# Performance work log

Measured on AMD Instinct MI355X. Metric: run time of the kernel, lower is better.

The kernel has to match this reference:

```python
import jax, jax.numpy as jnp
import numpy as np

NUM_CLASSES = 2
THRESHOLD = 0.35
NEGPOS_RATIO = 7
VARIANCES = (0.1, 0.2)
B, P, O = 64, 16800, 64  # batch, num_priors, num_objs per image


def point_form(pr):
    # cxcywh -> xyxy
    return jnp.concatenate([pr[:, :2] - pr[:, 2:] / 2, pr[:, :2] + pr[:, 2:] / 2], axis=1)


def jaccard(a, b):
    # a: [A,4] xyxy, b: [Bx,4] xyxy -> IoU [A,Bx]
    lt = jnp.maximum(a[:, None, :2], b[None, :, :2])
    rb = jnp.minimum(a[:, None, 2:], b[None, :, 2:])
    wh = jnp.clip(rb - lt, 0.0)
    inter = wh[..., 0] * wh[..., 1]
    area_a = ((a[:, 2] - a[:, 0]) * (a[:, 3] - a[:, 1]))[:, None]
    area_b = ((b[:, 2] - b[:, 0]) * (b[:, 3] - b[:, 1]))[None, :]
    return inter / (area_a + area_b - inter)


def encode(matched, priors):
    # matched xyxy [P,4], priors cxcywh [P,4]
    g_cxcy = (matched[:, :2] + matched[:, 2:]) / 2 - priors[:, :2]
    g_cxcy = g_cxcy / (VARIANCES[0] * priors[:, 2:])
    g_wh = (matched[:, 2:] - matched[:, :2]) / priors[:, 2:]
    g_wh = jnp.log(g_wh) / VARIANCES[1]
    return jnp.concatenate([g_cxcy, g_wh], axis=1)


def encode_landm(matched, priors):
    # matched [P,10] -> [P,5,2]
    m = matched.reshape(-1, 5, 2)
    g = (m - priors[:, None, :2]) / (VARIANCES[0] * priors[:, None, 2:])
    return g.reshape(-1, 10)


def match_one(truths, labels, landms, priors):
    # truths [O,4], labels [O], landms [O,10]
    overlaps = jaccard(truths, point_form(priors))  # [O,P]
    best_prior_overlap = overlaps.max(axis=1)       # per-gt best IoU
    best_prior_idx = overlaps.argmax(axis=1)
    valid_gt = best_prior_overlap >= 0.2
    best_truth_overlap = overlaps.max(axis=0)       # per-prior best IoU
    best_truth_idx = overlaps.argmax(axis=0)
    # index_fill(2) only for valid gts (best_prior_idx_filter)
    bto = best_truth_overlap.at[best_prior_idx].set(
        jnp.where(valid_gt, 2.0, best_truth_overlap[best_prior_idx]))
    # ensure every gt keeps its best prior
    bti = best_truth_idx.at[best_prior_idx].set(jnp.arange(truths.shape[0]))
    matches = truths[bti]                  # [P,4]
    conf = labels[bti]                     # [P]
    conf = jnp.where(bto < THRESHOLD, 0.0, conf)
    loc = encode(matches, priors)
    landm = encode_landm(landms[bti], priors)
    return loc, conf, landm


def smooth_l1_sum(x, mask):
    ax = jnp.abs(x)
    v = jnp.where(ax < 1.0, 0.5 * ax * ax, ax - 0.5)
    return (v * mask).sum()


def setup_inputs() -> dict:
    key = jax.random.key(0)
    k1, k2, k3, k4, k5, k6, k7, k8 = jax.random.split(key, 8)
    loc_data = jax.random.normal(k1, (B, P, 4), jnp.float32)
    conf_data = jax.random.normal(k2, (B, P, NUM_CLASSES), jnp.float32)
    landm_data = jax.random.normal(k3, (B, P, 10), jnp.float32)
    # priors: cx,cy in (0,1), w,h in (0.02,0.22)
    cxy = jax.random.uniform(k4, (P, 2), jnp.float32)
    wh = jax.random.uniform(k5, (P, 2), jnp.float32) * 0.2 + 0.02
    priors = jnp.concatenate([cxy, wh], axis=1)
    # targets: valid corner boxes + landmarks + label in {1,-1}
    xy1 = jax.random.uniform(k6, (B, O, 2), jnp.float32) * 0.6
    bwh = jax.random.uniform(k7, (B, O, 2), jnp.float32) * 0.3 + 0.05
    boxes = jnp.concatenate([xy1, xy1 + bwh], axis=-1)
    lms = jax.random.uniform(k8, (B, O, 10), jnp.float32)
    lab = jnp.where(jax.random.uniform(jax.random.fold_in(key, 9), (B, O, 1)) < 0.3, -1.0, 1.0)
    targets = jnp.concatenate([boxes, lms, lab], axis=-1)
    return {"loc_data": loc_data, "conf_data": conf_data, "landm_data": landm_data,
            "priors": priors, "targets": targets}


def reference(loc_data, conf_data, landm_data, priors, targets):
    num = loc_data.shape[0]
    num_priors = priors.shape[0]
    truths = targets[:, :, :4]
    landms = targets[:, :, 4:14]
    labels = targets[:, :, -1]
    loc_t, conf_t, landm_t = jax.vmap(match_one, in_axes=(0, 0, 0, None))(
        truths, labels, landms, priors)  # [B,P,4], [B,P], [B,P,10]

    # landmark loss over conf_t > 0
    pos1 = conf_t > 0
    num_pos_landm = pos1.astype(jnp.int32).sum(axis=1, keepdims=True)
    N1 = jnp.maximum(num_pos_landm.sum().astype(jnp.float32), 1.0)
    loss_landm = smooth_l1_sum(landm_data - landm_t, pos1[..., None].astype(landm_data.dtype))

    # localization loss over conf_t != 0 ; conf_t[pos] = 1
    pos = conf_t != 0
    conf_t01 = jnp.where(pos, 1, 0)  # int {0,1}
    loss_l = smooth_l1_sum(loc_data - loc_t, pos[..., None].astype(loc_data.dtype))

    # hard negative mining on per-prior CE loss (global-max log_sum_exp, as in source)
    batch_conf = conf_data.reshape(-1, NUM_CLASSES)
    x_max = batch_conf.max()
    lse = jnp.log(jnp.exp(batch_conf - x_max).sum(axis=1, keepdims=True)) + x_max
    gathered = jnp.take_along_axis(batch_conf, conf_t01.reshape(-1, 1), axis=1)
    loss_c = (lse - gathered).reshape(num, -1)  # [B,P]; positives NOT zeroed (as in source)
    loss_idx = jnp.argsort(-loss_c, axis=1)
    idx_rank = jnp.argsort(loss_idx, axis=1)
    num_pos = pos.astype(jnp.int32).sum(axis=1, keepdims=True)  # [B,1]
    num_neg = jnp.minimum(NEGPOS_RATIO * num_pos, num_priors - 1)
    neg = idx_rank < num_neg  # [B,P]
    neg_pos = pos | neg

    # cross-entropy (sum) over selected pos+neg priors
    logp = jax.nn.log_softmax(conf_data, axis=-1)  # [B,P,C]
    ce = -jnp.take_along_axis(logp, conf_t01[..., None], axis=-1)[..., 0]
    loss_c_final = (ce * neg_pos.astype(ce.dtype)).sum()

    N = jnp.maximum(num_pos.sum().astype(jnp.float32), 1.0)
    return (loss_l / N, loss_c_final / N, loss_landm / N1)
```

## Files before the change

kernel.cpp:

```cpp
#include <hip/hip_runtime.h>
#include <math.h>

#define BN 64
#define PN 16800
#define ON 64
#define THRESH 0.35f
#define NEGPOS 7
#define GX 66
#define NBLK (BN * GX)
#define GXB 17
#define NBT (BN * GXB)
#define PT 4
#define TG 4
#define PSPLIT 2
#define PHALF 8400
#define NBP2 (BN * 16 * PSPLIT)
#define NBINS 4096
#define MAXM 4096
#define TAILT 104

struct GAcc {
  unsigned ticket;
  float sl, slm, sc;
  int np, np1;
  unsigned pad0, pad1;
};

__device__ __forceinline__ unsigned f2key(float f) {
  unsigned u = __float_as_uint(f);
  return (u & 0x80000000u) ? ~u : (u | 0x80000000u);
}
__device__ __forceinline__ float key2f(unsigned k) {
  unsigned u = (k & 0x80000000u) ? (k & 0x7FFFFFFFu) : ~k;
  return __uint_as_float(u);
}
__device__ __forceinline__ float sl1(float d) {
  float a = fabsf(d);
  return (a < 1.f) ? 0.5f * a * a : a - 0.5f;
}

__global__ void k_match2(const float* __restrict__ priors,
                         const float* __restrict__ targets,
                         float* __restrict__ bto, int* __restrict__ bti,
                         unsigned long long* __restrict__ bpp,
                         GAcc* __restrict__ gacc) {
  int bid = blockIdx.x;
  int tid = threadIdx.x;

  if (bid < NBT) {
    int b = bid / GXB;
    int slab = bid - b * GXB;
    int base = slab * 1024 + tid;
    if (bid == 0 && tid < 8) ((unsigned*)gacc)[tid] = 0;

    __shared__ float4 tbox[ON];
    __shared__ float tarea[ON];
    if (tid < ON) {
      const float* tg = &targets[((long)b * ON + tid) * 15];
      float4 bx = make_float4(tg[0], tg[1], tg[2], tg[3]);
      tbox[tid] = bx;
      tarea[tid] = (bx.z - bx.x) * (bx.w - bx.y);
    }
    __syncthreads();

    float px1[PT], py1[PT], px2[PT], py2[PT], ab[PT];
    bool val[PT];
#pragma unroll
    for (int i = 0; i < PT; i++) {
      int p = base + 256 * i;
      val[i] = p < PN;
      float4 pr = reinterpret_cast<const float4*>(priors)[val[i] ? p : base];
      px1[i] = pr.x - pr.z * 0.5f; py1[i] = pr.y - pr.w * 0.5f;
      px2[i] = pr.x + pr.z * 0.5f; py2[i] = pr.y + pr.w * 0.5f;
      ab[i] = (px2[i] - px1[i]) * (py2[i] - py1[i]);
    }
    float bi[PT], bu[PT]; int id[PT];
#pragma unroll
    for (int i = 0; i < PT; i++) { bi[i] = -1.f; bu[i] = 1.f; id[i] = 0; }

#pragma unroll 4
    for (int t = 0; t < ON; t++) {
      float4 a = tbox[t];
      float aa = tarea[t];
#pragma unroll
      for (int i = 0; i < PT; i++) {
        float lx = fmaxf(a.x, px1[i]), ly = fmaxf(a.y, py1[i]);
        float rx = fminf(a.z, px2[i]), ry = fminf(a.w, py2[i]);
        float w = fmaxf(rx - lx, 0.f), h = fmaxf(ry - ly, 0.f);
        float inter = w * h;
        float uni = aa + ab[i] - inter;
        if (inter * bu[i] > bi[i] * uni) { bi[i] = inter; bu[i] = uni; id[i] = t; }
      }
    }
#pragma unroll
    for (int i = 0; i < PT; i++) {
      if (val[i]) {
        int p = base + 256 * i;
        bto[(long)b * PN + p] = bi[i] / bu[i];
        bti[(long)b * PN + p] = id[i];
      }
    }
  } else {
    int id2 = bid - NBT;
    int b = id2 >> 5;
    int rest = id2 & 31;
    int g = rest >> 1;
    int h = rest & 1;
    int t0 = g * TG;
    float ax1[TG], ay1[TG], ax2[TG], ay2[TG], area_a[TG];
#pragma unroll
    for (int i = 0; i < TG; i++) {
      const float* tg = &targets[((long)b * ON + t0 + i) * 15];
      ax1[i] = tg[0]; ay1[i] = tg[1]; ax2[i] = tg[2]; ay2[i] = tg[3];
      area_a[i] = (ax2[i] - ax1[i]) * (ay2[i] - ay1[i]);
    }
    float bi[TG], bu[TG]; int bp[TG];
#pragma unroll
    for (int i = 0; i < TG; i++) { bi[i] = -1.f; bu[i] = 1.f; bp[i] = 0x7FFFFFFF; }
    int pend = (h + 1) * PHALF;
    for (int p = h * PHALF + tid; p < pend; p += 256) {
      float4 pr = reinterpret_cast<const float4*>(priors)[p];
      float px1 = pr.x - pr.z * 0.5f, py1 = pr.y - pr.w * 0.5f;
      float px2 = pr.x + pr.z * 0.5f, py2 = pr.y + pr.w * 0.5f;
      float area_b = (px2 - px1) * (py2 - py1);
#pragma unroll
      for (int i = 0; i < TG; i++) {
        float lx = fmaxf(ax1[i], px1), ly = fmaxf(ay1[i], py1);
        float rx = fminf(ax2[i], px2), ry = fminf(ay2[i], py2);
        float w = fmaxf(rx - lx, 0.f), h2 = fmaxf(ry - ly, 0.f);
        float inter = w * h2;
        float uni = area_a[i] + area_b - inter;
        if (inter * bu[i] > bi[i] * uni) { bi[i] = inter; bu[i] = uni; bp[i] = p; }
      }
    }
#pragma unroll
    for (int off = 1; off < 64; off <<= 1) {
#pragma unroll
      for (int i = 0; i < TG; i++) {
        float oi = __shfl_xor(bi[i], off), ou = __shfl_xor(bu[i], off);
        int op = __shfl_xor(bp[i], off);
        float a = oi * bu[i], c = bi[i] * ou;
        if (a > c || (a == c && op < bp[i])) { bi[i] = oi; bu[i] = ou; bp[i] = op; }
      }
    }
    __shared__ float si[TG][4], su[TG][4];
    __shared__ int spx[TG][4];
    int w = tid >> 6;
    if ((tid & 63) == 0) {
#pragma unroll
      for (int i = 0; i < TG; i++) { si[i][w] = bi[i]; su[i][w] = bu[i]; spx[i][w] = bp[i]; }
    }
    __syncthreads();
    if (tid < TG) {
      float fi = si[tid][0], fu = su[tid][0]; int fp = spx[tid][0];
      for (int ww = 1; ww < 4; ww++) {
        float a = si[tid][ww] * fu, c = fi * su[tid][ww];
        if (a > c || (a == c && spx[tid][ww] < fp)) { fi = si[tid][ww]; fu = su[tid][ww]; fp = spx[tid][ww]; }
      }
      float q = fi / fu;
      unsigned long long key = ((unsigned long long)f2key(q) << 32) | (unsigned)(~fp);
      bpp[((long)b * ON + t0 + tid) * PSPLIT + h] = key;
    }
  }
}

__global__ void k_encode(const float* __restrict__ loc_data,
                         const float* __restrict__ conf_data,
                         const float* __restrict__ landm_data,
                         const float* __restrict__ priors,
                         const float* __restrict__ targets,
                         const float* __restrict__ bto, const int* __restrict__ bti,
                         const unsigned long long* __restrict__ bpp,
                         float* __restrict__ lossc, unsigned char* __restrict__ posf,
                         float* __restrict__ part_l, float* __restrict__ part_lm,
                         int* __restrict__ np_part, int* __restrict__ np1_part) {
  int b = blockIdx.y;
  int p = blockIdx.x * 256 + threadIdx.x;
  int bid = b * GX + blockIdx.x;
  __shared__ float4 tgs4[ON * 15 / 4];
  __shared__ int ovr[256];
  float* tgs = (float*)tgs4;
  if (threadIdx.x < ON * 15 / 4)
    tgs4[threadIdx.x] = reinterpret_cast<const float4*>(targets + (long)b * ON * 15)[threadIdx.x];
  ovr[threadIdx.x] = -1;
  __syncthreads();
  if (threadIdx.x < ON) {
    int t = threadIdx.x;
    unsigned long long v0 = bpp[((long)b * ON + t) * PSPLIT];
    unsigned long long v1 = bpp[((long)b * ON + t) * PSPLIT + 1];
    unsigned long long best = v0 > v1 ? v0 : v1;
    float q = key2f((unsigned)(best >> 32));
    int qp = (int)(~(unsigned)best);
    int s0 = blockIdx.x * 256;
    if (qp >= s0 && qp < s0 + 256) {
      int valid = (q >= 0.2f) ? 1 : 0;
      atomicMax(&ovr[qp - s0], (t << 1) | valid);
    }
  }
  __syncthreads();

  float sum_l = 0.f, sum_lm = 0.f;
  int cp = 0, cp1 = 0;
  if (p < PN) {
    int t = bti[b * PN + p];
    float ov = bto[b * PN + p];
    int o = ovr[threadIdx.x];
    if (o >= 0) { t = o >> 1; if (o & 1) ov = 2.0f; }
    const float* tg = &tgs[t * 15];
    float label = tg[14];
    bool pos = ov >= THRESH;
    bool pos1 = pos && (label > 0.f);
    float4 pr = reinterpret_cast<const float4*>(priors)[p];
    if (pos) {
      float rz = 1.0f / pr.z, rw = 1.0f / pr.w;
      float m0 = tg[0], m1 = tg[1], m2 = tg[2], m3 = tg[3];
      float g0 = ((m0 + m2) * 0.5f - pr.x) * rz * 10.f;
      float g1 = ((m1 + m3) * 0.5f - pr.y) * rw * 10.f;
      float g2 = __logf((m2 - m0) * rz) * 5.f;
      float g3 = __logf((m3 - m1) * rw) * 5.f;
      const float* ld = &loc_data[((long)b * PN + p) * 4];
      sum_l = sl1(ld[0] - g0) + sl1(ld[1] - g1) + sl1(ld[2] - g2) + sl1(ld[3] - g3);
      cp = 1;
      if (pos1) {
        const float* lm = &landm_data[((long)b * PN + p) * 10];
#pragma unroll
        for (int i = 0; i < 5; i++) {
          float gx = (tg[4 + 2 * i] - pr.x) * rz * 10.f;
          float gy = (tg[5 + 2 * i] - pr.y) * rw * 10.f;
          sum_lm += sl1(lm[2 * i] - gx) + sl1(lm[2 * i + 1] - gy);
        }
        cp1 = 1;
      }
    }
    float2 c2 = reinterpret_cast<const float2*>(conf_data)[(long)b * PN + p];
    float m = fmaxf(c2.x, c2.y);
    float lse = m + __logf(__expf(c2.x - m) + __expf(c2.y - m));
    lossc[b * PN + p] = lse - (pos ? c2.y : c2.x);
    posf[b * PN + p] = pos ? 1 : 0;
  }
  for (int off = 32; off; off >>= 1) {
    sum_l += __shfl_down(sum_l, off);
    sum_lm += __shfl_down(sum_lm, off);
    cp += __shfl_down(cp, off);
    cp1 += __shfl_down(cp1, off);
  }
  __shared__ float sl4[4], slm4[4];
  __shared__ int sp4[4], sp14[4];
  int w = threadIdx.x >> 6;
  if ((threadIdx.x & 63) == 0) { sl4[w] = sum_l; slm4[w] = sum_lm; sp4[w] = cp; sp14[w] = cp1; }
  __syncthreads();
  if (threadIdx.x == 0) {
    part_l[bid] = sl4[0] + sl4[1] + sl4[2] + sl4[3];
    part_lm[bid] = slm4[0] + slm4[1] + slm4[2] + slm4[3];
    np_part[bid] = sp4[0] + sp4[1] + sp4[2] + sp4[3];
    np1_part[bid] = sp14[0] + sp14[1] + sp14[2] + sp14[3];
  }
}

__global__ void __launch_bounds__(1024) k_select(const float* __restrict__ lossc,
                                                 const unsigned char* __restrict__ posf,
                                                 const int* __restrict__ np_part,
                                                 const int* __restrict__ np1_part,
                                                 const float* __restrict__ part_l,
                                                 const float* __restrict__ part_lm,
                                                 GAcc* __restrict__ gacc,
                                                 float* __restrict__ out) {
  int b = blockIdx.x;
  int tid = threadIdx.x;
  int lane = tid & 63;
  int wv = tid >> 6;
  __shared__ unsigned hist[NBINS];
  __shared__ unsigned wtot[16];
  __shared__ float resv[MAXM];
  __shared__ int residx[MAXM];
  __shared__ int s_np, s_B, s_kp;
  __shared__ unsigned s_mc;
  const float* row = &lossc[(long)b * PN];
  const unsigned char* prow = &posf[(long)b * PN];

  if (tid == 0) s_np = 0;
  for (int i = tid; i < NBINS; i += 1024) hist[i] = 0;
  __syncthreads();
  if (tid < GX) atomicAdd(&s_np, np_part[b * GX + tid]);

  const float4* rf4 = reinterpret_cast<const float4*>(row);
  const uint4* pw4 = reinterpret_cast<const uint4*>(prow);
  bool hasTail = tid < TAILT;
  float vm[16];
  float vt[4];
  {
    float4 L0 = rf4[tid * 4], L1 = rf4[tid * 4 + 1], L2 = rf4[tid * 4 + 2], L3 = rf4[tid * 4 + 3];
    vm[0] = L0.x; vm[1] = L0.y; vm[2] = L0.z; vm[3] = L0.w;
    vm[4] = L1.x; vm[5] = L1.y; vm[6] = L1.z; vm[7] = L1.w;
    vm[8] = L2.x; vm[9] = L2.y; vm[10] = L2.z; vm[11] = L2.w;
    vm[12] = L3.x; vm[13] = L3.y; vm[14] = L3.z; vm[15] = L3.w;
  }
  unsigned pmask = 0;
  {
    uint4 W = pw4[tid];
    unsigned w0 = W.x, w1 = W.y, w2 = W.z, w3 = W.w;
#pragma unroll
    for (int j = 0; j < 4; j++) {
      pmask |= ((w0 >> (8 * j)) & 1u) << j;
      pmask |= ((w1 >> (8 * j)) & 1u) << (4 + j);
      pmask |= ((w2 >> (8 * j)) & 1u) << (8 + j);
      pmask |= ((w3 >> (8 * j)) & 1u) << (12 + j);
    }
  }
  unsigned tmask = 0;
  if (hasTail) {
    float4 Lt = rf4[4096 + tid];
    vt[0] = Lt.x; vt[1] = Lt.y; vt[2] = Lt.z; vt[3] = Lt.w;
    unsigned Wt = reinterpret_cast<const unsigned*>(prow)[4096 + tid];
#pragma unroll
    for (int j = 0; j < 4; j++) tmask |= ((Wt >> (8 * j)) & 1u) << j;
  } else {
    vt[0] = vt[1] = vt[2] = vt[3] = -1.f;
  }
  int bm[16], bt4[4];
#pragma unroll
  for (int j = 0; j < 16; j++) {
    int q = (int)(vm[j] * 256.0f);
    bm[j] = q < 0 ? 0 : (q > NBINS - 1 ? NBINS - 1 : q);
  }
#pragma unroll
  for (int j = 0; j < 4; j++) {
    int q = (int)(vt[j] * 256.0f);
    bt4[j] = q < 0 ? 0 : (q > NBINS - 1 ? NBINS - 1 : q);
  }
  __syncthreads();
  int np = s_np;
  int k = NEGPOS * np;
  if (k > PN - 1) k = PN - 1;
  bool haveNeg = (k > 0);

  int B = NBINS, kp = 0, m = 0;
  bool allB = false, fallback = false;
  if (haveNeg) {
#pragma unroll
    for (int j = 0; j < 16; j++) atomicAdd(&hist[bm[j]], 1u);
    if (hasTail) {
#pragma unroll
      for (int j = 0; j < 4; j++) atomicAdd(&hist[bt4[j]], 1u);
    }
    __syncthreads();
    int t4 = tid * 4;
    unsigned h0 = hist[t4], h1 = hist[t4 + 1], h2 = hist[t4 + 2], h3 = hist[t4 + 3];
    unsigned th = h0 + h1 + h2 + h3;
    unsigned v = th;
#pragma unroll
    for (int off = 1; off < 64; off <<= 1) {
      unsigned tv = (unsigned)__shfl_down((int)v, off);
      if (lane + off < 64) v += tv;
    }
    if (lane == 0) wtot[wv] = v;
    __syncthreads();
    unsigned add = 0;
    for (int w2 = wv + 1; w2 < 16; w2++) add += wtot[w2];
    unsigned S_t = v + add;
    unsigned S_next = S_t - th;
    if (S_t >= (unsigned)k && S_next < (unsigned)k) {
      unsigned run = S_next; int Bl; unsigned kpl;
      if (run + h3 >= (unsigned)k) { Bl = t4 + 3; kpl = k - run; }
      else { run += h3;
        if (run + h2 >= (unsigned)k) { Bl = t4 + 2; kpl = k - run; }
        else { run += h2;
          if (run + h1 >= (unsigned)k) { Bl = t4 + 1; kpl = k - run; }
          else { run += h1; Bl = t4; kpl = k - run; } } }
      s_B = Bl; s_kp = (int)kpl;
    }
    __syncthreads();
    B = s_B; kp = s_kp; m = (int)hist[B];
    allB = (kp == m);
    fallback = (!allB && m > MAXM);
  }

  float acc = 0.f;
  if (haveNeg && !allB && !fallback) {
    if (tid == 0) s_mc = 0;
    __syncthreads();
#pragma unroll
    for (int j = 0; j < 16; j++) {
      if (bm[j] == B) {
        unsigned slot = atomicAdd(&s_mc, 1u);
        resv[slot] = vm[j];
        residx[slot] = (tid * 16 + j) | (((pmask >> j) & 1u) ? 0x40000000 : 0);
      }
    }
    if (hasTail) {
#pragma unroll
      for (int j = 0; j < 4; j++) {
        if (bt4[j] == B) {
          unsigned slot = atomicAdd(&s_mc, 1u);
          resv[slot] = vt[j];
          residx[slot] = (16384 + tid * 4 + j) | (((tmask >> j) & 1u) ? 0x40000000 : 0);
        }
      }
    }
    __syncthreads();
    for (int i = tid; i < m; i += 1024) {
      float vi = resv[i];
      int pk = residx[i];
      int ii = pk & 0x3FFFFFFF;
      bool posi = (pk & 0x40000000) != 0;
      int rank = 0;
      for (int j = 0; j < m; j++) {
        float vj = resv[j];
        int ij = residx[j] & 0x3FFFFFFF;
        rank += (vj > vi || (vj == vi && ij < ii)) ? 1 : 0;
      }
      if (rank < kp && !posi) acc += vi;
    }
  }

  unsigned T = 0, R = 0, C = 0;
  if (fallback) {
    __shared__ unsigned s_lo, s_hi, fcnt[16];
    if (tid == 0) { s_lo = 0u; s_hi = 0xFFFFFFFFu; }
    __syncthreads();
    for (int it = 0; it < 32; it++) {
      unsigned lo = s_lo, hi = s_hi;
      unsigned mid = lo + ((hi - lo) >> 1) + ((hi - lo) & 1u);
      unsigned c = 0;
#pragma unroll
      for (int j = 0; j < 16; j++) c += (f2key(vm[j]) >= mid) ? 1u : 0u;
      if (hasTail) {
#pragma unroll
        for (int j = 0; j < 4; j++) c += (f2key(vt[j]) >= mid) ? 1u : 0u;
      }
#pragma unroll
      for (int o = 32; o; o >>= 1) c += (unsigned)__shfl_down((int)c, o);
      if (lane == 0) fcnt[wv] = c;
      __syncthreads();
      if (tid == 0) {
        unsigned tot = 0;
        for (int i = 0; i < 16; i++) tot += fcnt[i];
        if (tot >= (unsigned)k) s_lo = mid; else s_hi = mid - 1;
      }
      __syncthreads();
      if (s_lo >= s_hi) break;
    }
    T = s_lo;
    unsigned cg = 0, ce = 0;
#pragma unroll
    for (int j = 0; j < 16; j++) {
      unsigned key = f2key(vm[j]);
      cg += (key > T) ? 1u : 0u;
      ce += (key == T) ? 1u : 0u;
    }
    if (hasTail) {
#pragma unroll
      for (int j = 0; j < 4; j++) {
        unsigned key = f2key(vt[j]);
        cg += (key > T) ? 1u : 0u;
        ce += (key == T) ? 1u : 0u;
      }
    }
#pragma unroll
    for (int o = 32; o; o >>= 1) {
      cg += (unsigned)__shfl_down((int)cg, o);
      ce += (unsigned)__shfl_down((int)ce, o);
    }
    if (lane == 0) { fcnt[wv] = cg; wtot[wv] = ce; }
    __syncthreads();
    if (tid == 0) {
      unsigned tg2 = 0, te = 0;
      for (int i = 0; i < 16; i++) { tg2 += fcnt[i]; te += wtot[i]; }
      fcnt[0] = tg2; wtot[0] = te;
    }
    __syncthreads();
    C = wtot[0];
    R = (unsigned)k - fcnt[0];
    if (C != R && tid < 64) {
      unsigned running = 0;
      for (int base2 = 0; base2 < PN; base2 += 64) {
        int p = base2 + tid;
        bool tie = false, pos = false;
        float v2 = 0.f;
        if (p < PN) { v2 = row[p]; tie = (f2key(v2) == T); pos = prow[p] != 0; }
        unsigned long long mm = __ballot(tie);
        if (tie) {
          unsigned rank = running + (unsigned)__popcll(mm & ((1ull << tid) - 1));
          if (rank < R && !pos) acc += v2;
        }
        running += (unsigned)__popcll(mm);
      }
    }
  }

  unsigned ptc = 0;
#pragma unroll
  for (int j = 0; j < 16; j++) {
    float v2 = vm[j];
    bool pos = (pmask >> j) & 1u;
    if (pos) acc += v2;
    else if (haveNeg) {
      if (!fallback) {
        if (bm[j] > B || (bm[j] == B && allB)) acc += v2;
      } else {
        if (f2key(v2) > T) acc += v2;
      }
    }
    if (fallback && pos && f2key(v2) == T) ptc++;
  }
  if (hasTail) {
#pragma unroll
    for (int j = 0; j < 4; j++) {
      float v2 = vt[j];
      bool pos = (tmask >> j) & 1u;
      if (pos) acc += v2;
      else if (haveNeg) {
        if (!fallback) {
          if (bt4[j] > B || (bt4[j] == B && allB)) acc += v2;
        } else {
          if (f2key(v2) > T) acc += v2;
        }
      }
      if (fallback && pos && f2key(v2) == T) ptc++;
    }
  }
  for (int o = 32; o; o >>= 1) {
    acc += __shfl_down(acc, o);
    ptc += __shfl_down(ptc, o);
  }
  __shared__ float wsum[16];
  __shared__ unsigned wpt[16];
  if (lane == 0) { wsum[wv] = acc; wpt[wv] = ptc; }
  __syncthreads();

  __shared__ float s_rsl, s_rslm;
  __shared__ int s_rnp1;
  if (tid == 0) { s_rsl = 0.f; s_rslm = 0.f; s_rnp1 = 0; }
  __syncthreads();
  if (tid < GX) {
    atomicAdd(&s_rsl, part_l[b * GX + tid]);
    atomicAdd(&s_rslm, part_lm[b * GX + tid]);
    atomicAdd(&s_rnp1, np1_part[b * GX + tid]);
  }
  __syncthreads();

  if (tid == 0) {
    float tot = 0.f; unsigned pt = 0;
    for (int i = 0; i < 16; i++) { tot += wsum[i]; pt += wpt[i]; }
    if (fallback && C == R) tot += (float)(C - pt) * key2f(T);
    atomicAdd(&gacc->sc, tot);
    atomicAdd(&gacc->sl, s_rsl);
    atomicAdd(&gacc->slm, s_rslm);
    atomicAdd(&gacc->np, np);
    atomicAdd(&gacc->np1, s_rnp1);
  }
  __threadfence();
  __shared__ int lastF;
  if (tid == 0) lastF = (atomicAdd(&gacc->ticket, 1u) == (unsigned)(BN - 1)) ? 1 : 0;
  __syncthreads();
  if (lastF && tid == 0) {
    __threadfence();
    float sl = atomicAdd(&gacc->sl, 0.f);
    float slm = atomicAdd(&gacc->slm, 0.f);
    float sc = atomicAdd(&gacc->sc, 0.f);
    int tnp = atomicAdd(&gacc->np, 0);
    int tnp1 = atomicAdd(&gacc->np1, 0);
    float N = fmaxf((float)tnp, 1.f);
    float N1 = fmaxf((float)tnp1, 1.f);
    out[0] = sl / N;
    out[1] = sc / N;
    out[2] = slm / N1;
  }
}

extern "C" void kernel_launch(void* const* d_in, const int* in_sizes, int n_in,
                              void* d_out, int out_size, void* d_ws, size_t ws_size,
                              hipStream_t stream) {
  const float* loc_data = (const float*)d_in[0];
  const float* conf_data = (const float*)d_in[1];
  const float* landm_data = (const float*)d_in[2];
  const float* priors = (const float*)d_in[3];
  const float* targets = (const float*)d_in[4];
  float* out = (float*)d_out;

  char* ws = (char*)d_ws;
  const size_t SZ = (size_t)BN * PN * 4;
  size_t off = 0;
  float* lossc = (float*)(ws + off); off += SZ;
  float* bto = (float*)(ws + off); off += SZ;
  int* bti = (int*)(ws + off); off += SZ;
  unsigned char* posf = (unsigned char*)(ws + off); off += (size_t)BN * PN;
  off = (off + 15) & ~(size_t)15;
  unsigned long long* bpp = (unsigned long long*)(ws + off);
  off += (size_t)BN * ON * PSPLIT * 8;
  float* part_l = (float*)(ws + off); off += NBLK * 4;
  float* part_lm = (float*)(ws + off); off += NBLK * 4;
  int* np_part = (int*)(ws + off); off += NBLK * 4;
  int* np1_part = (int*)(ws + off); off += NBLK * 4;
  GAcc* gacc = (GAcc*)(ws + off); off += sizeof(GAcc);

  dim3 gbp(GX, BN);

  k_match2<<<NBT + NBP2, 256, 0, stream>>>(priors, targets, bto, bti, bpp, gacc);
  k_encode<<<gbp, 256, 0, stream>>>(loc_data, conf_data, landm_data, priors, targets,
                                    bto, bti, bpp, lossc, posf,
                                    part_l, part_lm, np_part, np1_part);
  k_select<<<BN, 1024, 0, stream>>>(lossc, posf, np_part, np1_part, part_l, part_lm,
                                    gacc, out);
}
```

Baseline: 208.8 us.

## Bin priors into a spatial grid to prune IoU matching candidates

Adds a single-block prior sort into a 16x16 grid by center, per-image cell-to-target overlap masks, and a matching kernel that only evaluates IoU for gt/prior pairs in nearby cells. The per-prior best-truth result is packed into one byte (target id plus positive flag) instead of separate float and int arrays, which cuts global traffic. This removes most of the dense O×P IoU work but adds two extra serial launches, one of them a single-block kernel. It also relies on grid bounds from the maximum prior half-size and uses wave-wide mask unions, so some wavefronts may still scan many targets.

```diff
diff --git a/kernel.cpp b/kernel.cpp
--- a/kernel.cpp
+++ b/kernel.cpp
@@ -8,13 +8,9 @@
 #define NEGPOS 7
 #define GX 66
 #define NBLK (BN * GX)
-#define GXB 17
-#define NBT (BN * GXB)
-#define PT 4
-#define TG 4
-#define PSPLIT 2
-#define PHALF 8400
-#define NBP2 (BN * 16 * PSPLIT)
+#define NBP 1024
+#define NBTT (BN * GX)
+#define NCELL 256
 #define NBINS 4096
 #define MAXM 4096
 #define TAILT 104
@@ -39,127 +35,187 @@
   return (a < 1.f) ? 0.5f * a * a : a - 0.5f;
 }
 
-__global__ void k_match2(const float* __restrict__ priors,
-                         const float* __restrict__ targets,
-                         float* __restrict__ bto, int* __restrict__ bti,
-                         unsigned long long* __restrict__ bpp,
-                         GAcc* __restrict__ gacc) {
+__global__ void __launch_bounds__(1024) k_sort(const float* __restrict__ priors,
+                                               float4* __restrict__ sbox,
+                                               int* __restrict__ sorig,
+                                               int* __restrict__ scell,
+                                               int* __restrict__ inv,
+                                               int* __restrict__ cellOff,
+                                               unsigned* __restrict__ gmax,
+                                               GAcc* __restrict__ gacc) {
+  __shared__ unsigned cnt[NCELL];
+  __shared__ unsigned cur[NCELL];
+  __shared__ unsigned tmp[NCELL];
+  int tid = threadIdx.x;
+  if (tid < NCELL) cnt[tid] = 0;
+  if (tid == 0) { gmax[0] = 0u; gmax[1] = 0u; }
+  if (tid < 8) ((unsigned*)gacc)[tid] = 0;
+  __syncthreads();
+  float mw = 0.f, mh = 0.f;
+  for (int p = tid; p < PN; p += 1024) {
+    float4 pr = reinterpret_cast<const float4*>(priors)[p];
+    int cx = (int)(pr.x * 16.f); cx = cx < 0 ? 0 : (cx > 15 ? 15 : cx);
+    int cy = (int)(pr.y * 16.f); cy = cy < 0 ? 0 : (cy > 15 ? 15 : cy);
+    atomicAdd(&cnt[cy * 16 + cx], 1u);
+    mw = fmaxf(mw, pr.z * 0.5f);
+    mh = fmaxf(mh, pr.w * 0.5f);
+  }
+#pragma unroll
+  for (int off = 32; off; off >>= 1) {
+    mw = fmaxf(mw, __shfl_xor(mw, off));
+    mh = fmaxf(mh, __shfl_xor(mh, off));
+  }
+  if ((tid & 63) == 0) {
+    atomicMax(&gmax[0], __float_as_uint(mw));
+    atomicMax(&gmax[1], __float_as_uint(mh));
+  }
+  __syncthreads();
+  if (tid < NCELL) tmp[tid] = cnt[tid];
+  __syncthreads();
+  for (int off = 1; off < NCELL; off <<= 1) {
+    unsigned v = 0;
+    if (tid < NCELL && tid >= off) v = tmp[tid - off];
+    __syncthreads();
+    if (tid < NCELL) tmp[tid] += v;
+    __syncthreads();
+  }
+  if (tid < NCELL) {
+    unsigned excl = tmp[tid] - cnt[tid];
+    cur[tid] = excl;
+    cellOff[tid] = (int)excl;
+    if (tid == NCELL - 1) cellOff[NCELL] = (int)tmp[tid];
+  }
+  __syncthreads();
+  for (int p = tid; p < PN; p += 1024) {
+    float4 pr = reinterpret_cast<const float4*>(priors)[p];
+    int cx = (int)(pr.x * 16.f); cx = cx < 0 ? 0 : (cx > 15 ? 15 : cx);
+    int cy = (int)(pr.y * 16.f); cy = cy < 0 ? 0 : (cy > 15 ? 15 : cy);
+    int cell = cy * 16 + cx;
+    int s = (int)atomicAdd(&cur[cell], 1u);
+    float px1 = pr.x - pr.z * 0.5f, py1 = pr.y - pr.w * 0.5f;
+    float px2 = pr.x + pr.z * 0.5f, py2 = pr.y + pr.w * 0.5f;
+    sbox[s] = make_float4(px1, py1, px2, py2);
+    sorig[s] = p;
+    scell[s] = cell;
+    inv[p] = s;
+  }
+}
+
+__global__ void k_masks(const float* __restrict__ targets,
+                        const unsigned* __restrict__ gmax,
+                        unsigned long long* __restrict__ tmask) {
+  int b = blockIdx.x;
+  int tid = threadIdx.x;
+  __shared__ float4 tb[ON];
+  if (tid < ON) {
+    const float* tg = &targets[((long)b * ON + tid) * 15];
+    tb[tid] = make_float4(tg[0], tg[1], tg[2], tg[3]);
+  }
+  __syncthreads();
+  float MW = __uint_as_float(gmax[0]), MH = __uint_as_float(gmax[1]);
+  int cx = tid & 15, cy = tid >> 4;
+  float x0 = (float)(cx - 1) * 0.0625f - MW, x1 = (float)(cx + 2) * 0.0625f + MW;
+  float y0 = (float)(cy - 1) * 0.0625f - MH, y1 = (float)(cy + 2) * 0.0625f + MH;
+  unsigned long long m = 0ull;
+  for (int t = 0; t < ON; t++) {
+    float4 a = tb[t];
+    if (x0 < a.z && x1 > a.x && y0 < a.w && y1 > a.y) m |= (1ull << t);
+  }
+  tmask[b * NCELL + tid] = m;
+}
+
+__global__ void k_pair(const float* __restrict__ targets,
+                       const float4* __restrict__ sbox,
+                       const int* __restrict__ sorig,
+                       const int* __restrict__ scell,
+                       const int* __restrict__ cellOff,
+                       const unsigned* __restrict__ gmax,
+                       const unsigned long long* __restrict__ tmask,
+                       unsigned char* __restrict__ btpack,
+                       unsigned long long* __restrict__ bpp) {
   int bid = blockIdx.x;
   int tid = threadIdx.x;
 
-  if (bid < NBT) {
-    int b = bid / GXB;
-    int slab = bid - b * GXB;
-    int base = slab * 1024 + tid;
-    if (bid == 0 && tid < 8) ((unsigned*)gacc)[tid] = 0;
-
-    __shared__ float4 tbox[ON];
-    __shared__ float tarea[ON];
+  if (bid < NBP) {
+    int lane = tid & 63, wv = tid >> 6;
+    int b = bid >> 4;
+    int t = ((bid & 15) << 2) + wv;
+    const float* tg = &targets[((long)b * ON + t) * 15];
+    float ax1 = tg[0], ay1 = tg[1], ax2 = tg[2], ay2 = tg[3];
+    float aa = (ax2 - ax1) * (ay2 - ay1);
+    float MW = __uint_as_float(gmax[0]), MH = __uint_as_float(gmax[1]);
+    int xlo = (int)floorf((ax1 - MW) * 16.f) - 1; xlo = xlo < 0 ? 0 : (xlo > 15 ? 15 : xlo);
+    int xhi = (int)floorf((ax2 + MW) * 16.f) + 1; xhi = xhi < 0 ? 0 : (xhi > 15 ? 15 : xhi);
+    int ylo = (int)floorf((ay1 - MH) * 16.f) - 1; ylo = ylo < 0 ? 0 : (ylo > 15 ? 15 : ylo);
+    int yhi = (int)floorf((ay2 + MH) * 16.f) + 1; yhi = yhi < 0 ? 0 : (yhi > 15 ? 15 : yhi);
+    float bi = 0.f, bu = 1.f; int bp = 0;
+    for (int cy = ylo; cy <= yhi; cy++) {
+      int s0 = cellOff[cy * 16 + xlo];
+      int s1 = cellOff[cy * 16 + xhi + 1];
+      for (int s = s0 + lane; s < s1; s += 64) {
+        float4 pr = sbox[s];
+        int op = sorig[s];
+        float ab2 = (pr.z - pr.x) * (pr.w - pr.y);
+        float lx = fmaxf(ax1, pr.x), ly = fmaxf(ay1, pr.y);
+        float rx = fminf(ax2, pr.z), ry = fminf(ay2, pr.w);
+        float w = fmaxf(rx - lx, 0.f), h = fmaxf(ry - ly, 0.f);
+        float inter = w * h;
+        float uni = aa + ab2 - inter;
+        float A = inter * bu, C = bi * uni;
+        if (A > C || (A == C && op < bp)) { bi = inter; bu = uni; bp = op; }
+      }
+    }
+#pragma unroll
+    for (int off = 1; off < 64; off <<= 1) {
+      float oi = __shfl_xor(bi, off), ou = __shfl_xor(bu, off);
+      int op = __shfl_xor(bp, off);
+      float A = oi * bu, C = bi * ou;
+      if (A > C || (A == C && op < bp)) { bi = oi; bu = ou; bp = op; }
+    }
+    if (lane == 0) {
+      float q = bi / bu;
+      bpp[(long)b * ON + t] = ((unsigned long long)f2key(q) << 32) | (unsigned)(~bp);
+    }
+  } else {
+    int id2 = bid - NBP;
+    int b = id2 / GX;
+    int slab = id2 - b * GX;
+    int s = slab * 256 + tid;
+    bool valid = s < PN;
+    int sc = valid ? s : PN - 1;
+    __shared__ float4 tb[ON];
+    __shared__ float ta[ON];
     if (tid < ON) {
       const float* tg = &targets[((long)b * ON + tid) * 15];
       float4 bx = make_float4(tg[0], tg[1], tg[2], tg[3]);
-      tbox[tid] = bx;
-      tarea[tid] = (bx.z - bx.x) * (bx.w - bx.y);
-    }
-    __syncthreads();
-
-    float px1[PT], py1[PT], px2[PT], py2[PT], ab[PT];
-    bool val[PT];
-#pragma unroll
-    for (int i = 0; i < PT; i++) {
-      int p = base + 256 * i;
-      val[i] = p < PN;
-      float4 pr = reinterpret_cast<const float4*>(priors)[val[i] ? p : base];
-      px1[i] = pr.x - pr.z * 0.5f; py1[i] = pr.y - pr.w * 0.5f;
-      px2[i] = pr.x + pr.z * 0.5f; py2[i] = pr.y + pr.w * 0.5f;
-      ab[i] = (px2[i] - px1[i]) * (py2[i] - py1[i]);
-    }
-    float bi[PT], bu[PT]; int id[PT];
-#pragma unroll
-    for (int i = 0; i < PT; i++) { bi[i] = -1.f; bu[i] = 1.f; id[i] = 0; }
-
-#pragma unroll 4
-    for (int t = 0; t < ON; t++) {
-      float4 a = tbox[t];
-      float aa = tarea[t];
-#pragma unroll
-      for (int i = 0; i < PT; i++) {
-        float lx = fmaxf(a.x, px1[i]), ly = fmaxf(a.y, py1[i]);
-        float rx = fminf(a.z, px2[i]), ry = fminf(a.w, py2[i]);
-        float w = fmaxf(rx - lx, 0.f), h = fmaxf(ry - ly, 0.f);
-        float inter = w * h;
-        float uni = aa + ab[i] - inter;
-        if (inter * bu[i] > bi[i] * uni) { bi[i] = inter; bu[i] = uni; id[i] = t; }
-      }
-    }
-#pragma unroll
-    for (int i = 0; i < PT; i++) {
-      if (val[i]) {
-        int p = base + 256 * i;
-        bto[(long)b * PN + p] = bi[i] / bu[i];
-        bti[(long)b * PN + p] = id[i];
-      }
-    }
-  } else {
-    int id2 = bid - NBT;
-    int b = id2 >> 5;
-    int rest = id2 & 31;
-    int g = rest >> 1;
-    int h = rest & 1;
-    int t0 = g * TG;
-    float ax1[TG], ay1[TG], ax2[TG], ay2[TG], area_a[TG];
-#pragma unroll
-    for (int i = 0; i < TG; i++) {
-      const float* tg = &targets[((long)b * ON + t0 + i) * 15];
-      ax1[i] = tg[0]; ay1[i] = tg[1]; ax2[i] = tg[2]; ay2[i] = tg[3];
-      area_a[i] = (ax2[i] - ax1[i]) * (ay2[i] - ay1[i]);
-    }
-    float bi[TG], bu[TG]; int bp[TG];
-#pragma unroll
-    for (int i = 0; i < TG; i++) { bi[i] = -1.f; bu[i] = 1.f; bp[i] = 0x7FFFFFFF; }
-    int pend = (h + 1) * PHALF;
-    for (int p = h * PHALF + tid; p < pend; p += 256) {
-      float4 pr = reinterpret_cast<const float4*>(priors)[p];
-      float px1 = pr.x - pr.z * 0.5f, py1 = pr.y - pr.w * 0.5f;
-      float px2 = pr.x + pr.z * 0.5f, py2 = pr.y + pr.w * 0.5f;
-      float area_b = (px2 - px1) * (py2 - py1);
-#pragma unroll
-      for (int i = 0; i < TG; i++) {
-        float lx = fmaxf(ax1[i], px1), ly = fmaxf(ay1[i], py1);
-        float rx = fminf(ax2[i], px2), ry = fminf(ay2[i], py2);
-        float w = fmaxf(rx - lx, 0.f), h2 = fmaxf(ry - ly, 0.f);
-        float inter = w * h2;
-        float uni = area_a[i] + area_b - inter;
-        if (inter * bu[i] > bi[i] * uni) { bi[i] = inter; bu[i] = uni; bp[i] = p; }
-      }
-    }
-#pragma unroll
-    for (int off = 1; off < 64; off <<= 1) {
-#pragma unroll
-      for (int i = 0; i < TG; i++) {
-        float oi = __shfl_xor(bi[i], off), ou = __shfl_xor(bu[i], off);
-        int op = __shfl_xor(bp[i], off);
-        float a = oi * bu[i], c = bi[i] * ou;
-        if (a > c || (a == c && op < bp[i])) { bi[i] = oi; bu[i] = ou; bp[i] = op; }
-      }
-    }
-    __shared__ float si[TG][4], su[TG][4];
-    __shared__ int spx[TG][4];
-    int w = tid >> 6;
-    if ((tid & 63) == 0) {
-#pragma unroll
-      for (int i = 0; i < TG; i++) { si[i][w] = bi[i]; su[i][w] = bu[i]; spx[i][w] = bp[i]; }
-    }
-    __syncthreads();
-    if (tid < TG) {
-      float fi = si[tid][0], fu = su[tid][0]; int fp = spx[tid][0];
-      for (int ww = 1; ww < 4; ww++) {
-        float a = si[tid][ww] * fu, c = fi * su[tid][ww];
-        if (a > c || (a == c && spx[tid][ww] < fp)) { fi = si[tid][ww]; fu = su[tid][ww]; fp = spx[tid][ww]; }
-      }
-      float q = fi / fu;
-      unsigned long long key = ((unsigned long long)f2key(q) << 32) | (unsigned)(~fp);
-      bpp[((long)b * ON + t0 + tid) * PSPLIT + h] = key;
+      tb[tid] = bx;
+      ta[tid] = (bx.z - bx.x) * (bx.w - bx.y);
+    }
+    __syncthreads();
+    float4 pr = sbox[sc];
+    float ab2 = (pr.z - pr.x) * (pr.w - pr.y);
+    unsigned long long um = valid ? tmask[b * NCELL + scell[sc]] : 0ull;
+#pragma unroll
+    for (int off = 1; off < 64; off <<= 1) um |= __shfl_xor(um, off);
+    unsigned mlo = (unsigned)__builtin_amdgcn_readfirstlane((int)(unsigned)um);
+    unsigned mhi = (unsigned)__builtin_amdgcn_readfirstlane((int)(unsigned)(um >> 32));
+    unsigned long long m = ((unsigned long long)mhi << 32) | mlo;
+    float bi = 0.f, bu = 1.f; int id = 0;
+    while (m) {
+      int t = __builtin_ctzll(m);
+      m &= m - 1;
+      float4 a = tb[t];
+      float lx = fmaxf(a.x, pr.x), ly = fmaxf(a.y, pr.y);
+      float rx = fminf(a.z, pr.z), ry = fminf(a.w, pr.w);
+      float w = fmaxf(rx - lx, 0.f), h = fmaxf(ry - ly, 0.f);
+      float inter = w * h;
+      float uni = ta[t] + ab2 - inter;
+      if (inter * bu > bi * uni) { bi = inter; bu = uni; id = t; }
+    }
+    if (valid) {
+      float q = bi / bu;
+      unsigned char posb = (q >= THRESH) ? 1 : 0;
+      btpack[(long)b * PN + s] = (unsigned char)((id << 1) | posb);
     }
   }
 }
@@ -169,7 +225,8 @@
                          const float* __restrict__ landm_data,
                          const float* __restrict__ priors,
                          const float* __restrict__ targets,
-                         const float* __restrict__ bto, const int* __restrict__ bti,
+                         const unsigned char* __restrict__ btpack,
+                         const int* __restrict__ inv,
                          const unsigned long long* __restrict__ bpp,
                          float* __restrict__ lossc, unsigned char* __restrict__ posf,
                          float* __restrict__ part_l, float* __restrict__ part_lm,
@@ -186,9 +243,7 @@
   __syncthreads();
   if (threadIdx.x < ON) {
     int t = threadIdx.x;
-    unsigned long long v0 = bpp[((long)b * ON + t) * PSPLIT];
-    unsigned long long v1 = bpp[((long)b * ON + t) * PSPLIT + 1];
-    unsigned long long best = v0 > v1 ? v0 : v1;
+    unsigned long long best = bpp[(long)b * ON + t];
     float q = key2f((unsigned)(best >> 32));
     int qp = (int)(~(unsigned)best);
     int s0 = blockIdx.x * 256;
@@ -202,13 +257,13 @@
   float sum_l = 0.f, sum_lm = 0.f;
   int cp = 0, cp1 = 0;
   if (p < PN) {
-    int t = bti[b * PN + p];
-    float ov = bto[b * PN + p];
+    unsigned pk = btpack[(long)b * PN + inv[p]];
+    int t = (int)(pk >> 1);
+    bool pos = (pk & 1u) != 0;
     int o = ovr[threadIdx.x];
-    if (o >= 0) { t = o >> 1; if (o & 1) ov = 2.0f; }
+    if (o >= 0) { t = o >> 1; if (o & 1) pos = true; }
     const float* tg = &tgs[t * 15];
     float label = tg[14];
-    bool pos = ov >= THRESH;
     bool pos1 = pos && (label > 0.f);
     float4 pr = reinterpret_cast<const float4*>(priors)[p];
     if (pos) {
@@ -579,26 +634,32 @@
   float* out = (float*)d_out;
 
   char* ws = (char*)d_ws;
-  const size_t SZ = (size_t)BN * PN * 4;
   size_t off = 0;
-  float* lossc = (float*)(ws + off); off += SZ;
-  float* bto = (float*)(ws + off); off += SZ;
-  int* bti = (int*)(ws + off); off += SZ;
+  float* lossc = (float*)(ws + off); off += (size_t)BN * PN * 4;
+  unsigned char* btpack = (unsigned char*)(ws + off); off += (size_t)BN * PN;
   unsigned char* posf = (unsigned char*)(ws + off); off += (size_t)BN * PN;
   off = (off + 15) & ~(size_t)15;
-  unsigned long long* bpp = (unsigned long long*)(ws + off);
-  off += (size_t)BN * ON * PSPLIT * 8;
+  unsigned long long* bpp = (unsigned long long*)(ws + off); off += (size_t)BN * ON * 8;
   float* part_l = (float*)(ws + off); off += NBLK * 4;
   float* part_lm = (float*)(ws + off); off += NBLK * 4;
   int* np_part = (int*)(ws + off); off += NBLK * 4;
   int* np1_part = (int*)(ws + off); off += NBLK * 4;
+  float4* sbox = (float4*)(ws + off); off += (size_t)PN * 16;
+  int* sorig = (int*)(ws + off); off += (size_t)PN * 4;
+  int* scell = (int*)(ws + off); off += (size_t)PN * 4;
+  int* inv = (int*)(ws + off); off += (size_t)PN * 4;
+  int* cellOff = (int*)(ws + off); off += 260 * 4;
+  unsigned* gmax = (unsigned*)(ws + off); off += 16;
+  unsigned long long* tmask = (unsigned long long*)(ws + off); off += (size_t)BN * NCELL * 8;
   GAcc* gacc = (GAcc*)(ws + off); off += sizeof(GAcc);
 
+  k_sort<<<1, 1024, 0, stream>>>(priors, sbox, sorig, scell, inv, cellOff, gmax, gacc);
+  k_masks<<<BN, 256, 0, stream>>>(targets, gmax, tmask);
+  k_pair<<<NBP + NBTT, 256, 0, stream>>>(targets, sbox, sorig, scell, cellOff, gmax,
+                                         tmask, btpack, bpp);
   dim3 gbp(GX, BN);
-
-  k_match2<<<NBT + NBP2, 256, 0, stream>>>(priors, targets, bto, bti, bpp, gacc);
   k_encode<<<gbp, 256, 0, stream>>>(loc_data, conf_data, landm_data, priors, targets,
-                                    bto, bti, bpp, lossc, posf,
+                                    btpack, inv, bpp, lossc, posf,
                                     part_l, part_lm, np_part, np1_part);
   k_select<<<BN, 1024, 0, stream>>>(lossc, posf, np_part, np1_part, part_l, part_lm,
                                     gacc, out);
```

After: 226.5 us. +8.5%, slower.
